# Kernel optimization log

Measured on AMD Instinct MI355X. Metric: run time of the kernel, lower is better.

The kernel has to match this reference:

```python
import jax, jax.numpy as jnp
from jax import lax
import numpy as np

IMG = 224
NB = IMG // 8  # 28 blocks per spatial dim

# DCT-II (ortho) 8x8 basis matrix
_D = np.cos(np.pi * (2 * np.arange(8)[None, :] + 1) * np.arange(8)[:, None] / 16.0) * np.sqrt(2.0 / 8.0)
_D[0, :] *= 1.0 / np.sqrt(2.0)
DCT8 = jnp.asarray(_D, dtype=jnp.float32)


def _conv(x, w, b, s):
    y = lax.conv_general_dilated(x, w, (s, s), 'SAME', dimension_numbers=('NCHW', 'OIHW', 'NCHW'))
    return y + b[None, :, None, None]


def _pool7(h):  # adaptive avg pool 56x56 -> 7x7, flatten
    B = h.shape[0]
    return h.reshape(B, 64, 7, 8, 7, 8).mean(axis=(3, 5)).reshape(B, -1)


def setup_inputs() -> dict:
    key = jax.random.key(0)
    ks = jax.random.split(key, 16)
    r = jax.nn.initializers.normal(0.02)
    inp = {
        'x': jax.random.uniform(ks[0], (64, 3, IMG, IMG), jnp.float32),
        'w_stem': r(ks[1], (64, 3, 7, 7), jnp.float32), 'b_stem': jnp.zeros((64,), jnp.float32),
        'w1': r(ks[2], (128, 64, 3, 3), jnp.float32), 'b1': jnp.zeros((128,), jnp.float32),
        'w2': r(ks[3], (256, 128, 3, 3), jnp.float32), 'b2': jnp.zeros((256,), jnp.float32),
        'w3': r(ks[4], (512, 256, 3, 3), jnp.float32), 'b3': jnp.zeros((512,), jnp.float32),
        'wd1': r(ks[5], (32, 3, 3, 3), jnp.float32), 'bd1': jnp.zeros((32,), jnp.float32),
        'wd2': r(ks[6], (64, 32, 3, 3), jnp.float32), 'bd2': jnp.zeros((64,), jnp.float32),
        'wf1': r(ks[7], (32, 6, 3, 3), jnp.float32), 'bf1': jnp.zeros((32,), jnp.float32),
        'wf2': r(ks[8], (64, 32, 3, 3), jnp.float32), 'bf2': jnp.zeros((64,), jnp.float32),
        'W_freq': r(ks[9], (6272, 512), jnp.float32), 'b_freq': jnp.zeros((512,), jnp.float32),
        'W_fu1': r(ks[10], (1024, 1024), jnp.float32), 'b_fu1': jnp.zeros((1024,), jnp.float32),
        'W_fu2': r(ks[11], (1024, 512), jnp.float32), 'b_fu2': jnp.zeros((512,), jnp.float32),
        'W_cls': r(ks[12], (512, 2), jnp.float32), 'b_cls': jnp.zeros((2,), jnp.float32),
        'temp': 1.5 * jnp.ones((1,), jnp.float32),
    }
    return inp


def reference(x, w_stem, b_stem, w1, b1, w2, b2, w3, b3, wd1, bd1, wd2, bd2,
              wf1, bf1, wf2, bf2, W_freq, b_freq, W_fu1, b_fu1, W_fu2, b_fu2,
              W_cls, b_cls, temp):
    relu = jax.nn.relu
    B = x.shape[0]
    # --- CNN backbone (resnet18 surrogate): 4 stride-2 stages -> GAP 512 ---
    h = relu(_conv(x, w_stem, b_stem, 2))
    h = relu(_conv(h, w1, b1, 2))
    h = relu(_conv(h, w2, b2, 2))
    h = relu(_conv(h, w3, b3, 2))
    backbone_feat = h.mean(axis=(2, 3))  # [B, 512]
    # --- DCT branch: grayscale -> batched 8x8 block DCT-II ortho -> mean -> resize ---
    gray = (0.299 * x[:, 0] + 0.587 * x[:, 1] + 0.114 * x[:, 2]) * 255.0  # [B,224,224]
    blocks = gray.reshape(B, NB, 8, NB, 8).transpose(0, 1, 3, 2, 4)  # [B,28,28,8,8]
    dctb = jnp.einsum('ij,bmnjk,lk->bmnil', DCT8, blocks, DCT8)  # D @ blk @ D^T
    dct_img = dctb.mean(axis=(1, 2))  # [B,8,8]
    dct_img = jax.image.resize(dct_img, (B, IMG, IMG), 'bilinear')
    dct_in = jnp.broadcast_to(dct_img[:, None], (B, 3, IMG, IMG))
    hd = relu(_conv(dct_in, wd1, bd1, 2))
    hd = relu(_conv(hd, wd2, bd2, 2))  # [B,64,56,56]
    dct_pooled = _pool7(hd)  # [B,3136]
    # --- FFT branch: batched 2D FFT, interleaved real/imag per channel -> 6 ch ---
    f = jnp.fft.fft2(x)  # [B,3,224,224] complex
    fft_in = jnp.stack([f.real, f.imag], axis=2).reshape(B, 6, IMG, IMG).astype(x.dtype)
    hf = relu(_conv(fft_in, wf1, bf1, 2))
    hf = relu(_conv(hf, wf2, bf2, 2))
    fft_pooled = _pool7(hf)  # [B,3136]
    # --- fusion + classifier + temperature scaling ---
    freq = relu(jnp.concatenate([dct_pooled, fft_pooled], axis=1) @ W_freq + b_freq)
    comb = jnp.concatenate([backbone_feat, freq], axis=1)  # [B,1024]
    fused = relu(relu(comb @ W_fu1 + b_fu1) @ W_fu2 + b_fu2)
    logits = fused @ W_cls + b_cls
    calibrated = logits / temp
    return (logits, calibrated)
```

## Files before the change

kernel.cpp:

```cpp
#include <hip/hip_runtime.h>

#ifndef M_PI
#define M_PI 3.14159265358979323846
#endif


#define BATCH 64

typedef __bf16 bf16x8 __attribute__((ext_vector_type(8)));
typedef float f32x4 __attribute__((ext_vector_type(4)));

__device__ __forceinline__ unsigned short f2bf(float f) {
    unsigned u = __float_as_uint(f);
    u += 0x7FFF + ((u >> 16) & 1);
    return (unsigned short)(u >> 16);
}
__device__ __forceinline__ unsigned packsplit(float v) {
    unsigned short h = f2bf(v);
    float hf = __uint_as_float(((unsigned)h) << 16);
    unsigned short l = f2bf(v - hf);
    return (((unsigned)h) << 16) | (unsigned)l;
}

union U8frag { bf16x8 v; unsigned d[4]; };

__device__ __forceinline__ void unpack8(const unsigned* p, bf16x8& hi, bf16x8& lo) {
    uint4 a = *(const uint4*)p;
    uint4 b = *(const uint4*)(p + 4);
    U8frag H, L;
    H.d[0] = __builtin_amdgcn_perm(a.y, a.x, 0x07060302u);
    L.d[0] = __builtin_amdgcn_perm(a.y, a.x, 0x05040100u);
    H.d[1] = __builtin_amdgcn_perm(a.w, a.z, 0x07060302u);
    L.d[1] = __builtin_amdgcn_perm(a.w, a.z, 0x05040100u);
    H.d[2] = __builtin_amdgcn_perm(b.y, b.x, 0x07060302u);
    L.d[2] = __builtin_amdgcn_perm(b.y, b.x, 0x05040100u);
    H.d[3] = __builtin_amdgcn_perm(b.w, b.z, 0x07060302u);
    L.d[3] = __builtin_amdgcn_perm(b.w, b.z, 0x05040100u);
    hi = H.v; lo = L.v;
}

__device__ __forceinline__ bf16x8 bfneg(bf16x8 v) {
    U8frag a; a.v = v;
    a.d[0] ^= 0x80008000u; a.d[1] ^= 0x80008000u;
    a.d[2] ^= 0x80008000u; a.d[3] ^= 0x80008000u;
    return a.v;
}

__device__ __forceinline__ int swz_bx() {
    int bx = blockIdx.x;
    int nb = gridDim.x;
    if ((nb & 7) == 0) bx = (bx & 7) * (nb >> 3) + (bx >> 3);
    return bx;
}

__global__ void prep_w(const float* __restrict__ w, unsigned* __restrict__ dst,
                       int Co, int Ci) {
    int idx = blockIdx.x * 256 + threadIdx.x;
    int tot = Co * Ci * 9;
    if (idx >= tot) return;
    int k9 = idx % 9;
    int rest = idx / 9;
    int ci = rest % Ci, co = rest / Ci;
    dst[((size_t)k9 * Co + co) * Ci + ci] = packsplit(w[idx]);
}

__global__ void prep_wstem(const float* __restrict__ w, unsigned* __restrict__ dst) {
    int idx = blockIdx.x * 256 + threadIdx.x;
    if (idx >= 64 * 224) return;
    int co = idx / 224, k = idx % 224;
    int ci = k & 3, kx = (k >> 2) & 7, ky = k >> 5;
    float v = 0.f;
    if (ci < 3 && kx < 7)
        v = w[((co * 3 + ci) * 7 + ky) * 7 + kx];
    dst[idx] = packsplit(v);
}

__global__ void pack_f32(const float* __restrict__ src, unsigned* __restrict__ dst, int n) {
    int i = blockIdx.x * 256 + threadIdx.x;
    if (i < n) dst[i] = packsplit(src[i]);
}

__global__ __launch_bounds__(256)
void conv3x3s2_mfma(const unsigned* __restrict__ inP, const unsigned* __restrict__ wP,
                    const float* __restrict__ bias,
                    unsigned* __restrict__ outPk, float* __restrict__ outF0,
                    float* __restrict__ outF1,
                    int Ci, int Co, int Hin, int Win, int Hout, int Wout,
                    int NTOT, int ciPer, int mode) {
    __shared__ unsigned sA[128 * 36];
    __shared__ unsigned sB[64 * 36];
    const int tid = threadIdx.x;
    const int wv = tid >> 6, lane = tid & 63;
    const int ciBeg = blockIdx.z * ciPer;
    const int coT0 = blockIdx.y * 128;
    const int HWin = Hin * Win, HWout = Hout * Wout;
    const int bx = swz_bx();

    const int nG = bx * 64 + (tid >> 2);
    const int kqB = tid & 3;
    int bb = 0, yy = 0, xx = 0;
    bool nval = nG < NTOT;
    if (nval) {
        bb = nG / HWout;
        int rem = nG - bb * HWout;
        yy = rem / Wout;
        xx = rem - yy * Wout;
    }
    const unsigned baseImg = (unsigned)bb * Ci * HWin;
    const int coA = tid >> 1, halfA = tid & 1;

    f32x4 acc[2][4];
#pragma unroll
    for (int s = 0; s < 2; s++)
#pragma unroll
        for (int t = 0; t < 4; t++) acc[s][t] = (f32x4){0.f, 0.f, 0.f, 0.f};

    for (int k9 = 0; k9 < 9; k9++) {
        int ky = k9 / 3, kx = k9 - ky * 3;
        int iy = 2 * yy + ky, ix = 2 * xx + kx;
        bool bval = nval && iy < Hin && ix < Win;
        unsigned off0 = baseImg + (unsigned)iy * Win + (unsigned)ix;
        const unsigned* wbase = wP + ((size_t)k9 * Co + coT0 + coA) * Ci + ciBeg + halfA * 16;

        for (int c0 = 0; c0 < ciPer; c0 += 32) {
            __syncthreads();
            {
                const uint4* g = (const uint4*)(wbase + c0);
                uint4 v0 = g[0], v1 = g[1], v2 = g[2], v3 = g[3];
                uint4* d = (uint4*)(sA + coA * 36 + halfA * 16);
                d[0] = v0; d[1] = v1; d[2] = v2; d[3] = v3;
            }
            {
                unsigned u[8];
                const unsigned cbase = off0 + (unsigned)(ciBeg + c0 + kqB * 8) * HWin;
#pragma unroll
                for (int j = 0; j < 8; j++)
                    u[j] = bval ? inP[cbase + (unsigned)j * HWin] : 0u;
                uint4* d = (uint4*)(sB + (tid >> 2) * 36 + kqB * 8);
                uint4 w0; w0.x = u[0]; w0.y = u[1]; w0.z = u[2]; w0.w = u[3];
                uint4 w1; w1.x = u[4]; w1.y = u[5]; w1.z = u[6]; w1.w = u[7];
                d[0] = w0; d[1] = w1;
            }
            __syncthreads();

            bf16x8 ah[2], al[2], bh[4], bl[4];
            const int m = lane & 15, q = lane >> 4;
#pragma unroll
            for (int s = 0; s < 2; s++)
                unpack8(sA + (wv * 32 + s * 16 + m) * 36 + q * 8, ah[s], al[s]);
#pragma unroll
            for (int t = 0; t < 4; t++)
                unpack8(sB + (t * 16 + m) * 36 + q * 8, bh[t], bl[t]);

#pragma unroll
            for (int s = 0; s < 2; s++)
#pragma unroll
                for (int t = 0; t < 4; t++)
                    acc[s][t] = __builtin_amdgcn_mfma_f32_16x16x32_bf16(ah[s], bh[t], acc[s][t], 0, 0, 0);
#pragma unroll
            for (int s = 0; s < 2; s++)
#pragma unroll
                for (int t = 0; t < 4; t++)
                    acc[s][t] = __builtin_amdgcn_mfma_f32_16x16x32_bf16(ah[s], bl[t], acc[s][t], 0, 0, 0);
#pragma unroll
            for (int s = 0; s < 2; s++)
#pragma unroll
                for (int t = 0; t < 4; t++)
                    acc[s][t] = __builtin_amdgcn_mfma_f32_16x16x32_bf16(al[s], bh[t], acc[s][t], 0, 0, 0);
        }
    }

    const int m = lane & 15, q = lane >> 4;
#pragma unroll
    for (int t = 0; t < 4; t++) {
        int n_g = bx * 64 + t * 16 + m;
        if (n_g >= NTOT) continue;
        int b = n_g / HWout;
        int rem = n_g - b * HWout;
        size_t nb = (size_t)b * Co * HWout + rem;
#pragma unroll
        for (int s = 0; s < 2; s++) {
            int co_l = wv * 32 + s * 16 + q * 4;
#pragma unroll
            for (int r = 0; r < 4; r++) {
                int co_g = coT0 + co_l + r;
                float v = acc[s][t][r];
                size_t addr = nb + (size_t)co_g * HWout;
                if (mode == 0) {
                    v += bias[co_g];
                    v = v > 0.f ? v : 0.f;
                    outPk[addr] = packsplit(v);
                } else {
                    (blockIdx.z == 0 ? outF0 : outF1)[addr] = v;
                }
            }
        }
    }
}

__global__ __launch_bounds__(256)
void conv3x3s2_mfma64(const unsigned* __restrict__ inP, const unsigned* __restrict__ wP,
                      const float* __restrict__ bias, float* __restrict__ outF,
                      int Hin, int Win, int Hout, int Wout, int NTOT) {
    const int Ci = 32;
    __shared__ unsigned sA[64 * 36];
    __shared__ unsigned sB[64 * 36];
    const int tid = threadIdx.x;
    const int wv = tid >> 6, lane = tid & 63;
    const int HWin = Hin * Win, HWout = Hout * Wout;
    const int bx = swz_bx();

    const int nG = bx * 64 + (tid >> 2);
    const int kq = tid & 3;
    int bb = 0, yy = 0, xx = 0;
    bool nval = nG < NTOT;
    if (nval) {
        bb = nG / HWout;
        int rem = nG - bb * HWout;
        yy = rem / Wout;
        xx = rem - yy * Wout;
    }
    const unsigned baseImg = (unsigned)bb * Ci * HWin;
    const int ch = wv & 1, nh = wv >> 1;

    f32x4 acc[2][2];
#pragma unroll
    for (int s = 0; s < 2; s++)
#pragma unroll
        for (int t = 0; t < 2; t++) acc[s][t] = (f32x4){0.f, 0.f, 0.f, 0.f};

    for (int k9 = 0; k9 < 9; k9++) {
        int ky = k9 / 3, kx = k9 - ky * 3;
        int iy = 2 * yy + ky, ix = 2 * xx + kx;
        bool bval = nval && iy < Hin && ix < Win;
        unsigned off0 = baseImg + (unsigned)iy * Win + (unsigned)ix;
        __syncthreads();
        {
            const unsigned* g = wP + ((size_t)k9 * 64 + (tid >> 2)) * Ci + kq * 8;
            uint4 v0 = *(const uint4*)g;
            uint4 v1 = *(const uint4*)(g + 4);
            uint4* d = (uint4*)(sA + (tid >> 2) * 36 + kq * 8);
            d[0] = v0; d[1] = v1;
        }
        {
            unsigned u[8];
            const unsigned cbase = off0 + (unsigned)(kq * 8) * HWin;
#pragma unroll
            for (int j = 0; j < 8; j++)
                u[j] = bval ? inP[cbase + (unsigned)j * HWin] : 0u;
            uint4* d = (uint4*)(sB + (tid >> 2) * 36 + kq * 8);
            uint4 w0; w0.x = u[0]; w0.y = u[1]; w0.z = u[2]; w0.w = u[3];
            uint4 w1; w1.x = u[4]; w1.y = u[5]; w1.z = u[6]; w1.w = u[7];
            d[0] = w0; d[1] = w1;
        }
        __syncthreads();

        bf16x8 ah[2], al[2], bh[2], bl[2];
        const int m = lane & 15, q = lane >> 4;
#pragma unroll
        for (int s = 0; s < 2; s++)
            unpack8(sA + (ch * 32 + s * 16 + m) * 36 + q * 8, ah[s], al[s]);
#pragma unroll
        for (int t = 0; t < 2; t++)
            unpack8(sB + (nh * 32 + t * 16 + m) * 36 + q * 8, bh[t], bl[t]);

#pragma unroll
        for (int s = 0; s < 2; s++)
#pragma unroll
            for (int t = 0; t < 2; t++)
                acc[s][t] = __builtin_amdgcn_mfma_f32_16x16x32_bf16(ah[s], bh[t], acc[s][t], 0, 0, 0);
#pragma unroll
        for (int s = 0; s < 2; s++)
#pragma unroll
            for (int t = 0; t < 2; t++)
                acc[s][t] = __builtin_amdgcn_mfma_f32_16x16x32_bf16(ah[s], bl[t], acc[s][t], 0, 0, 0);
#pragma unroll
        for (int s = 0; s < 2; s++)
#pragma unroll
            for (int t = 0; t < 2; t++)
                acc[s][t] = __builtin_amdgcn_mfma_f32_16x16x32_bf16(al[s], bh[t], acc[s][t], 0, 0, 0);
    }

    const int m = lane & 15, q = lane >> 4;
#pragma unroll
    for (int t = 0; t < 2; t++) {
        int n_g = bx * 64 + nh * 32 + t * 16 + m;
        if (n_g >= NTOT) continue;
        int b = n_g / HWout;
        int rem = n_g - b * HWout;
        size_t nb = (size_t)b * 64 * HWout + rem;
#pragma unroll
        for (int s = 0; s < 2; s++) {
            int co0 = ch * 32 + s * 16 + q * 4;
#pragma unroll
            for (int r = 0; r < 4; r++) {
                int co = co0 + r;
                float v = acc[s][t][r] + bias[co];
                outF[nb + (size_t)co * HWout] = v > 0.f ? v : 0.f;
            }
        }
    }
}

__global__ __launch_bounds__(256)
void conv7x7s2_mfma(const unsigned* __restrict__ inP, const unsigned* __restrict__ wP,
                    const float* __restrict__ bias, unsigned* __restrict__ outPk,
                    int NTOT) {
    __shared__ unsigned sA[64 * 36];
    __shared__ unsigned sB[64 * 36];
    const int tid = threadIdx.x;
    const int wv = tid >> 6, lane = tid & 63;
    const int HWout = 112 * 112;
    const int bx = swz_bx();

    const int nG = bx * 64 + (tid >> 2);
    const int kq = tid & 3;
    bool nval = nG < NTOT;
    int bb = 0, yy = 0, xx = 0;
    if (nval) {
        bb = nG / HWout;
        int rem = nG - bb * HWout;
        yy = rem / 112;
        xx = rem - yy * 112;
    }
    const int iy0 = 2 * yy - 2, ix0 = 2 * xx - 2;
    const unsigned baseImg = (unsigned)bb * 3 * 50176;
    const int ch = wv & 1, nh = wv >> 1;

    f32x4 acc[2][2];
#pragma unroll
    for (int s = 0; s < 2; s++)
#pragma unroll
        for (int t = 0; t < 2; t++) acc[s][t] = (f32x4){0.f, 0.f, 0.f, 0.f};

#pragma unroll
    for (int kyc = 0; kyc < 7; kyc++) {
        const int c0 = kyc * 32;
        const int iy = iy0 + kyc;
        const bool iyv = nval && iy >= 0 && iy < 224;
        __syncthreads();
        {
            const unsigned* g = wP + (tid >> 2) * 224 + c0 + kq * 8;
            uint4 v0 = *(const uint4*)g;
            uint4 v1 = *(const uint4*)(g + 4);
            uint4* d = (uint4*)(sA + (tid >> 2) * 36 + kq * 8);
            d[0] = v0; d[1] = v1;
        }
        {
            unsigned u[8];
            const unsigned rowbase = baseImg + (unsigned)(iy * 224);
#pragma unroll
            for (int j = 0; j < 8; j++) {
                int ci = j & 3;
                int kx = kq * 2 + (j >> 2);
                int ix = ix0 + kx;
                bool v = iyv && ci < 3 && kx < 7 && ix >= 0 && ix < 224;
                u[j] = v ? inP[rowbase + (unsigned)(ci * 50176 + ix)] : 0u;
            }
            uint4* d = (uint4*)(sB + (tid >> 2) * 36 + kq * 8);
            uint4 w0; w0.x = u[0]; w0.y = u[1]; w0.z = u[2]; w0.w = u[3];
            uint4 w1; w1.x = u[4]; w1.y = u[5]; w1.z = u[6]; w1.w = u[7];
            d[0] = w0; d[1] = w1;
        }
        __syncthreads();

        bf16x8 ah[2], al[2], bh[2], bl[2];
        const int m = lane & 15, q = lane >> 4;
#pragma unroll
        for (int s = 0; s < 2; s++)
            unpack8(sA + (ch * 32 + s * 16 + m) * 36 + q * 8, ah[s], al[s]);
#pragma unroll
        for (int t = 0; t < 2; t++)
            unpack8(sB + (nh * 32 + t * 16 + m) * 36 + q * 8, bh[t], bl[t]);

#pragma unroll
        for (int s = 0; s < 2; s++)
#pragma unroll
            for (int t = 0; t < 2; t++)
                acc[s][t] = __builtin_amdgcn_mfma_f32_16x16x32_bf16(ah[s], bh[t], acc[s][t], 0, 0, 0);
#pragma unroll
        for (int s = 0; s < 2; s++)
#pragma unroll
            for (int t = 0; t < 2; t++)
                acc[s][t] = __builtin_amdgcn_mfma_f32_16x16x32_bf16(ah[s], bl[t], acc[s][t], 0, 0, 0);
#pragma unroll
        for (int s = 0; s < 2; s++)
#pragma unroll
            for (int t = 0; t < 2; t++)
                acc[s][t] = __builtin_amdgcn_mfma_f32_16x16x32_bf16(al[s], bh[t], acc[s][t], 0, 0, 0);
    }

    const int m = lane & 15, q = lane >> 4;
#pragma unroll
    for (int t = 0; t < 2; t++) {
        int n_g = bx * 64 + nh * 32 + t * 16 + m;
        if (n_g >= NTOT) continue;
        int b = n_g / HWout;
        int rem = n_g - b * HWout;
        size_t nb = (size_t)b * 64 * HWout + rem;
#pragma unroll
        for (int s = 0; s < 2; s++) {
            int co0 = ch * 32 + s * 16 + q * 4;
#pragma unroll
            for (int r = 0; r < 4; r++) {
                int co = co0 + r;
                float v = acc[s][t][r] + bias[co];
                v = v > 0.f ? v : 0.f;
                outPk[nb + (size_t)co * HWout] = packsplit(v);
            }
        }
    }
}

__global__ void make_dft(unsigned* __restrict__ wre, unsigned* __restrict__ wim) {
    int idx = blockIdx.x * 256 + threadIdx.x;
    if (idx >= 224 * 224) return;
    int j = idx / 224, k = idx % 224;
    int m = (j * k) % 224;
    double a = -2.0 * M_PI * (double)m / 224.0;
    wre[idx] = packsplit((float)cos(a));
    wim[idx] = packsplit((float)sin(a));
}

__global__ void make_wsum(const float* __restrict__ wd1, float* __restrict__ wsum) {
    int idx = threadIdx.x;
    if (idx >= 288) return;
    int o = idx / 9, k = idx % 9;
    wsum[idx] = wd1[o * 27 + k] + wd1[o * 27 + 9 + k] + wd1[o * 27 + 18 + k];
}

__global__ __launch_bounds__(64)
void dft_mfma_s1(const unsigned* __restrict__ wre, const unsigned* __restrict__ wim,
                 const unsigned* __restrict__ xpk,
                 unsigned* __restrict__ ttre, unsigned* __restrict__ ttim) {
    const int z = blockIdx.z;
    const int m0 = blockIdx.x * 32, n0 = blockIdx.y * 32;
    const int lane = threadIdx.x;
    const int ml = lane & 15, q = lane >> 4;
    const unsigned* xb = xpk + (size_t)z * 50176;

    f32x4 cre[2][2], cim[2][2];
#pragma unroll
    for (int s = 0; s < 2; s++)
#pragma unroll
        for (int t = 0; t < 2; t++) { cre[s][t] = (f32x4){0,0,0,0}; cim[s][t] = (f32x4){0,0,0,0}; }

    for (int k0 = 0; k0 < 224; k0 += 32) {
        bf16x8 arh[2], arl[2], aih[2], ail[2], bh[2], bl[2];
#pragma unroll
        for (int s = 0; s < 2; s++) {
            int row = m0 + s * 16 + ml;
            unpack8(wre + row * 224 + k0 + q * 8, arh[s], arl[s]);
            unpack8(wim + row * 224 + k0 + q * 8, aih[s], ail[s]);
        }
#pragma unroll
        for (int t = 0; t < 2; t++)
            unpack8(xb + (n0 + t * 16 + ml) * 224 + k0 + q * 8, bh[t], bl[t]);

#pragma unroll
        for (int s = 0; s < 2; s++)
#pragma unroll
            for (int t = 0; t < 2; t++) {
                cre[s][t] = __builtin_amdgcn_mfma_f32_16x16x32_bf16(arh[s], bh[t], cre[s][t], 0, 0, 0);
                cre[s][t] = __builtin_amdgcn_mfma_f32_16x16x32_bf16(arh[s], bl[t], cre[s][t], 0, 0, 0);
                cre[s][t] = __builtin_amdgcn_mfma_f32_16x16x32_bf16(arl[s], bh[t], cre[s][t], 0, 0, 0);
                cim[s][t] = __builtin_amdgcn_mfma_f32_16x16x32_bf16(aih[s], bh[t], cim[s][t], 0, 0, 0);
                cim[s][t] = __builtin_amdgcn_mfma_f32_16x16x32_bf16(aih[s], bl[t], cim[s][t], 0, 0, 0);
                cim[s][t] = __builtin_amdgcn_mfma_f32_16x16x32_bf16(ail[s], bh[t], cim[s][t], 0, 0, 0);
            }
    }

    unsigned* tre = ttre + (size_t)z * 50176;
    unsigned* tim = ttim + (size_t)z * 50176;
#pragma unroll
    for (int s = 0; s < 2; s++)
#pragma unroll
        for (int t = 0; t < 2; t++)
#pragma unroll
            for (int r = 0; r < 4; r++) {
                int m = m0 + s * 16 + q * 4 + r;
                int n = n0 + t * 16 + ml;
                tre[m * 224 + n] = packsplit(cre[s][t][r]);
                tim[m * 224 + n] = packsplit(cim[s][t][r]);
            }
}

__global__ __launch_bounds__(64)
void dft_mfma_s2(const unsigned* __restrict__ wre, const unsigned* __restrict__ wim,
                 const unsigned* __restrict__ ttre, const unsigned* __restrict__ ttim,
                 float* __restrict__ fft_in) {
    const int z = blockIdx.z;
    const int m0 = blockIdx.x * 32, n0 = blockIdx.y * 32;
    const int lane = threadIdx.x;
    const int ml = lane & 15, q = lane >> 4;
    const unsigned* tre = ttre + (size_t)z * 50176;
    const unsigned* tim = ttim + (size_t)z * 50176;

    f32x4 cre[2][2], cim[2][2];
#pragma unroll
    for (int s = 0; s < 2; s++)
#pragma unroll
        for (int t = 0; t < 2; t++) { cre[s][t] = (f32x4){0,0,0,0}; cim[s][t] = (f32x4){0,0,0,0}; }

    for (int k0 = 0; k0 < 224; k0 += 32) {
        bf16x8 arh[2], arl[2], aih[2], ail[2];
        bf16x8 brh[2], brl[2], bih[2], bil[2];
#pragma unroll
        for (int s = 0; s < 2; s++) {
            int row = m0 + s * 16 + ml;
            unpack8(wre + row * 224 + k0 + q * 8, arh[s], arl[s]);
            unpack8(wim + row * 224 + k0 + q * 8, aih[s], ail[s]);
        }
#pragma unroll
        for (int t = 0; t < 2; t++) {
            int row = n0 + t * 16 + ml;
            unpack8(tre + row * 224 + k0 + q * 8, brh[t], brl[t]);
            unpack8(tim + row * 224 + k0 + q * 8, bih[t], bil[t]);
        }

#pragma unroll
        for (int t = 0; t < 2; t++) {
            bf16x8 nih = bfneg(bih[t]);
            bf16x8 nil = bfneg(bil[t]);
#pragma unroll
            for (int s = 0; s < 2; s++) {
                cre[s][t] = __builtin_amdgcn_mfma_f32_16x16x32_bf16(arh[s], brh[t], cre[s][t], 0, 0, 0);
                cre[s][t] = __builtin_amdgcn_mfma_f32_16x16x32_bf16(arh[s], brl[t], cre[s][t], 0, 0, 0);
                cre[s][t] = __builtin_amdgcn_mfma_f32_16x16x32_bf16(arl[s], brh[t], cre[s][t], 0, 0, 0);
                cre[s][t] = __builtin_amdgcn_mfma_f32_16x16x32_bf16(aih[s], nih, cre[s][t], 0, 0, 0);
                cre[s][t] = __builtin_amdgcn_mfma_f32_16x16x32_bf16(aih[s], nil, cre[s][t], 0, 0, 0);
                cre[s][t] = __builtin_amdgcn_mfma_f32_16x16x32_bf16(ail[s], nih, cre[s][t], 0, 0, 0);
                cim[s][t] = __builtin_amdgcn_mfma_f32_16x16x32_bf16(arh[s], bih[t], cim[s][t], 0, 0, 0);
                cim[s][t] = __builtin_amdgcn_mfma_f32_16x16x32_bf16(arh[s], bil[t], cim[s][t], 0, 0, 0);
                cim[s][t] = __builtin_amdgcn_mfma_f32_16x16x32_bf16(arl[s], bih[t], cim[s][t], 0, 0, 0);
                cim[s][t] = __builtin_amdgcn_mfma_f32_16x16x32_bf16(aih[s], brh[t], cim[s][t], 0, 0, 0);
                cim[s][t] = __builtin_amdgcn_mfma_f32_16x16x32_bf16(aih[s], brl[t], cim[s][t], 0, 0, 0);
                cim[s][t] = __builtin_amdgcn_mfma_f32_16x16x32_bf16(ail[s], brh[t], cim[s][t], 0, 0, 0);
            }
        }
    }

    const int b_loc = z / 3, c = z % 3;
    float* yre = fft_in + (size_t)(b_loc * 6 + 2 * c) * 50176;
    float* yim = yre + 50176;
#pragma unroll
    for (int s = 0; s < 2; s++)
#pragma unroll
        for (int t = 0; t < 2; t++)
#pragma unroll
            for (int r = 0; r < 4; r++) {
                int m = m0 + s * 16 + q * 4 + r;
                int n = n0 + t * 16 + ml;
                yre[m * 224 + n] = cre[s][t][r];
                yim[m * 224 + n] = cim[s][t][r];
            }
}

template <int CO_BLK, int TH, int TW, int CI_CHUNK, bool PACK>
__global__ __launch_bounds__(CO_BLK * TH)
void conv3x3_s2(const float* __restrict__ in, const float* __restrict__ w,
                const float* __restrict__ bias, float* __restrict__ out,
                int Ci, int Co, int Hin, int Win, int Hout, int Wout) {
    constexpr int IN_H = 2 * TH + 1;
    constexpr int IN_W = 2 * TW + 1;
    constexpr int IN_WP = 32;
    constexpr int WSTR = (CI_CHUNK * 9) | 1;
    __shared__ __align__(16) float s_in[CI_CHUNK][IN_H][IN_WP];
    __shared__ float s_w[CO_BLK * WSTR];

    const int tid = threadIdx.x;
    const int tiles_x = Wout / TW;
    const int tile = blockIdx.x;
    const int ty0 = (tile / tiles_x) * TH;
    const int tx0 = (tile % tiles_x) * TW;
    const int cog = blockIdx.y;
    const int b = blockIdx.z;
    const int co = tid % CO_BLK;
    const int ty = tid / CO_BLK;
    const int co_g = cog * CO_BLK + co;

    float acc[TW];
#pragma unroll
    for (int i = 0; i < TW; i++) acc[i] = 0.f;

    const float* in_b = in + (size_t)b * Ci * Hin * Win;
    const int iy0 = 2 * ty0, ix0 = 2 * tx0;

    for (int ci0 = 0; ci0 < Ci; ci0 += CI_CHUNK) {
        for (int idx = tid; idx < CI_CHUNK * IN_H * IN_W; idx += CO_BLK * TH) {
            int ci = idx / (IN_H * IN_W);
            int rem = idx % (IN_H * IN_W);
            int r = rem / IN_W, cc = rem % IN_W;
            int gy = iy0 + r, gx = ix0 + cc;
            float v = 0.f;
            if (gy < Hin && gx < Win)
                v = in_b[(size_t)(ci0 + ci) * Hin * Win + (size_t)gy * Win + gx];
            s_in[ci][r][cc] = v;
        }
        for (int idx = tid; idx < CO_BLK * CI_CHUNK * 9; idx += CO_BLK * TH) {
            int c = idx / (CI_CHUNK * 9);
            int k = idx % (CI_CHUNK * 9);
            s_w[c * WSTR + k] = w[((size_t)(cog * CO_BLK + c) * Ci + ci0) * 9 + k];
        }
        __syncthreads();

#pragma unroll
        for (int ci = 0; ci < CI_CHUNK; ci++) {
            float wr[9];
#pragma unroll
            for (int k = 0; k < 9; k++) wr[k] = s_w[co * WSTR + ci * 9 + k];
#pragma unroll
            for (int ky = 0; ky < 3; ky++) {
                float r[IN_WP];
                const float4* rowp = (const float4*)&s_in[ci][2 * ty + ky][0];
#pragma unroll
                for (int qq = 0; qq < IN_WP / 4; qq++) {
                    float4 v = rowp[qq];
                    r[4 * qq] = v.x; r[4 * qq + 1] = v.y; r[4 * qq + 2] = v.z; r[4 * qq + 3] = v.w;
                }
#pragma unroll
                for (int kx = 0; kx < 3; kx++) {
                    float wv = wr[ky * 3 + kx];
#pragma unroll
                    for (int xq = 0; xq < TW; xq++) acc[xq] += r[2 * xq + kx] * wv;
                }
            }
        }
        __syncthreads();
    }
    float bb = bias[co_g];
    size_t obase = ((size_t)b * Co + co_g) * Hout * Wout + (size_t)(ty0 + ty) * Wout + tx0;
#pragma unroll
    for (int xq = 0; xq < TW; xq++) {
        float v = acc[xq] + bb;
        v = v > 0.f ? v : 0.f;
        if (PACK)
            ((unsigned*)out)[obase + xq] = packsplit(v);
        else
            out[obase + xq] = v;
    }
}

__device__ __forceinline__ float dct_coef(int u, int i) {
    if (u == 0) return 0.35355339059327373f;
    return 0.5f * cosf((float)M_PI * (float)((2 * i + 1) * u) / 16.0f);
}

__global__ __launch_bounds__(256)
void dct_partial(const float* __restrict__ x, float* __restrict__ accum) {
    __shared__ float red[256];
    const int b = blockIdx.x, g = blockIdx.y;
    const int tid = threadIdx.x;
    const int ij = tid & 63;
    const int grp = tid >> 6;
    const int i = ij >> 3, j = ij & 7;
    const float* xb = x + (size_t)b * 3 * 50176;
    float s = 0.f;
    for (int blk = g * 4 + grp; blk < 784; blk += 48) {
        int m = blk / 28, n = blk % 28;
        size_t o = (size_t)(m * 8 + i) * 224 + n * 8 + j;
        s += 0.299f * xb[o] + 0.587f * xb[50176 + o] + 0.114f * xb[2 * 50176 + o];
    }
    red[tid] = s;
    __syncthreads();
    if (tid < 64)
        atomicAdd(&accum[b * 64 + tid],
                  red[tid] + red[tid + 64] + red[tid + 128] + red[tid + 192]);
}

__global__ __launch_bounds__(64)
void dct_final(const float* __restrict__ accum, float* __restrict__ dct_out) {
    __shared__ float Mb[64];
    const int b = blockIdx.x, tid = threadIdx.x;
    Mb[tid] = accum[b * 64 + tid] * (255.f / 784.f);
    __syncthreads();
    int u = tid >> 3, v = tid & 7;
    float acc = 0.f;
#pragma unroll
    for (int i2 = 0; i2 < 8; i2++) {
        float du = dct_coef(u, i2);
#pragma unroll
        for (int j2 = 0; j2 < 8; j2++) acc += du * Mb[i2 * 8 + j2] * dct_coef(v, j2);
    }
    dct_out[b * 64 + tid] = acc;
}

__global__ void resize_bilinear(const float* __restrict__ dct, float* __restrict__ out) {
    int idx = blockIdx.x * 256 + threadIdx.x;
    if (idx >= BATCH * 224 * 224) return;
    int b = idx / (224 * 224);
    int rem = idx % (224 * 224);
    int y = rem / 224, xx = rem % 224;
    float sy = fminf(fmaxf((y + 0.5f) * (1.f / 28.f) - 0.5f, 0.f), 7.f);
    float sx = fminf(fmaxf((xx + 0.5f) * (1.f / 28.f) - 0.5f, 0.f), 7.f);
    int y0 = (int)floorf(sy); if (y0 > 6) y0 = 6;
    int x0 = (int)floorf(sx); if (x0 > 6) x0 = 6;
    float ty = sy - y0, tx = sx - x0;
    const float* M = dct + b * 64;
    float v00 = M[y0 * 8 + x0], v01 = M[y0 * 8 + x0 + 1];
    float v10 = M[(y0 + 1) * 8 + x0], v11 = M[(y0 + 1) * 8 + x0 + 1];
    out[idx] = (1.f - ty) * ((1.f - tx) * v00 + tx * v01) + ty * ((1.f - tx) * v10 + tx * v11);
}

__global__ void pool7(const float* __restrict__ h, float* __restrict__ out,
                      int col_base, int n) {
    int idx = blockIdx.x * 256 + threadIdx.x;
    if (idx >= n) return;
    int b = idx / (64 * 49);
    int rem = idx % (64 * 49);
    int c = rem / 49;
    int ij = rem % 49;
    int i = ij / 7, j = ij % 7;
    const float* hp = h + ((size_t)(b * 64 + c)) * 56 * 56 + (size_t)i * 8 * 56 + j * 8;
    float s = 0.f;
#pragma unroll
    for (int r = 0; r < 8; r++)
#pragma unroll
        for (int q = 0; q < 8; q++) s += hp[r * 56 + q];
    out[(size_t)b * 6272 + col_base + c * 49 + ij] = s * (1.f / 64.f);
}

__global__ void gap2_kernel(const float* __restrict__ ha, const float* __restrict__ hb,
                            const float* __restrict__ bias, float* __restrict__ comb,
                            int nwaves) {
    int gt = blockIdx.x * blockDim.x + threadIdx.x;
    int wid = gt >> 6;
    int lane = gt & 63;
    if (wid >= nwaves) return;
    int b = wid / 512, c = wid % 512;
    const float* pa = ha + (size_t)wid * 196;
    const float* pb = hb + (size_t)wid * 196;
    float bbv = bias[c];
    float s = 0.f;
    for (int i = lane; i < 196; i += 64) {
        float v = pa[i] + pb[i] + bbv;
        s += v > 0.f ? v : 0.f;
    }
#pragma unroll
    for (int off = 32; off > 0; off >>= 1) s += __shfl_down(s, off);
    if (lane == 0) comb[(size_t)b * 1024 + c] = s * (1.f / 196.f);
}

__global__ __launch_bounds__(256)
void gemm64_part(const float* __restrict__ A, const float* __restrict__ Bm,
                 float* __restrict__ part, int N, int K, int KC) {
    __shared__ __align__(16) float sA[16][68];
    __shared__ __align__(16) float sB[16][68];
    const int tid = threadIdx.x;
    const int n0 = blockIdx.x * 64;
    const int kbase = blockIdx.z * KC;
    const int tr = (tid >> 4) << 2;
    const int tc = (tid & 15) << 2;
    float acc[4][4];
#pragma unroll
    for (int r = 0; r < 4; r++)
#pragma unroll
        for (int c = 0; c < 4; c++) acc[r][c] = 0.f;

    for (int k0 = 0; k0 < KC; k0 += 16) {
        for (int i = tid; i < 1024; i += 256) {
            int m = i >> 4, k = i & 15;
            sA[k][m] = A[(size_t)m * K + kbase + k0 + k];
        }
        for (int i = tid; i < 1024; i += 256) {
            int k = i >> 6, n = i & 63;
            sB[k][n] = Bm[(size_t)(kbase + k0 + k) * N + n0 + n];
        }
        __syncthreads();
#pragma unroll
        for (int k = 0; k < 16; k++) {
            float4 a = *(const float4*)&sA[k][tr];
            float4 bv = *(const float4*)&sB[k][tc];
            float av[4] = {a.x, a.y, a.z, a.w};
            float bb[4] = {bv.x, bv.y, bv.z, bv.w};
#pragma unroll
            for (int r = 0; r < 4; r++)
#pragma unroll
                for (int c = 0; c < 4; c++) acc[r][c] += av[r] * bb[c];
        }
        __syncthreads();
    }
    float* dst = part + (size_t)blockIdx.z * 64 * N;
#pragma unroll
    for (int r = 0; r < 4; r++) {
        float4 v; v.x = acc[r][0]; v.y = acc[r][1]; v.z = acc[r][2]; v.w = acc[r][3];
        *(float4*)&dst[(size_t)(tr + r) * N + n0 + tc] = v;
    }
}

__global__ void reduce_bias_relu(const float* __restrict__ part, const float* __restrict__ bias,
                                 float* __restrict__ dst, int N, int nz,
                                 int dstStride, int dstOff) {
    int idx = blockIdx.x * 256 + threadIdx.x;
    if (idx >= BATCH * N) return;
    int b = idx / N, n = idx % N;
    float s = bias[n];
    for (int z = 0; z < nz; z++) s += part[((size_t)z * BATCH + b) * N + n];
    dst[(size_t)b * dstStride + dstOff + n] = s > 0.f ? s : 0.f;
}

__global__ void logits_kernel(const float* __restrict__ fused, const float* __restrict__ Wc,
                              const float* __restrict__ bcls, const float* __restrict__ temp,
                              float* __restrict__ out) {
    int idx = threadIdx.x;
    if (idx >= 128) return;
    int b = idx >> 1, n = idx & 1;
    float s = bcls[n];
    const float* f = fused + (size_t)b * 512;
    for (int k = 0; k < 512; k++) s += f[k] * Wc[k * 2 + n];
    out[idx] = s;
    out[128 + idx] = s / temp[0];
}

static inline int ceil8(int n) { return (n + 7) & ~7; }

extern "C" void kernel_launch(void* const* d_in, const int* in_sizes, int n_in,
                              void* d_out, int out_size, void* d_ws, size_t ws_size,
                              hipStream_t stream) {
    const float* x      = (const float*)d_in[0];
    const float* w_stem = (const float*)d_in[1];
    const float* b_stem = (const float*)d_in[2];
    const float* w1 = (const float*)d_in[3];   const float* b1 = (const float*)d_in[4];
    const float* w2 = (const float*)d_in[5];   const float* b2 = (const float*)d_in[6];
    const float* w3 = (const float*)d_in[7];   const float* b3 = (const float*)d_in[8];
    const float* wd1 = (const float*)d_in[9];  const float* bd1 = (const float*)d_in[10];
    const float* wd2 = (const float*)d_in[11]; const float* bd2 = (const float*)d_in[12];
    const float* wf1 = (const float*)d_in[13]; const float* bf1 = (const float*)d_in[14];
    const float* wf2 = (const float*)d_in[15]; const float* bf2 = (const float*)d_in[16];
    const float* W_freq = (const float*)d_in[17]; const float* b_freq = (const float*)d_in[18];
    const float* W_fu1  = (const float*)d_in[19]; const float* b_fu1  = (const float*)d_in[20];
    const float* W_fu2  = (const float*)d_in[21]; const float* b_fu2  = (const float*)d_in[22];
    const float* W_cls  = (const float*)d_in[23]; const float* b_cls  = (const float*)d_in[24];
    const float* temp   = (const float*)d_in[25];
    float* ws = (float*)d_ws;
    float* out = (float*)d_out;

    const size_t IMG2 = 224 * 224;

    size_t oWRE  = 0;
    size_t oWIM  = oWRE + IMG2;
    size_t oWSUM = oWIM + IMG2;
    size_t oDCT  = oWSUM + 288;
    size_t oDIMG = oDCT + (size_t)BATCH * 64;
    size_t oFREQIN  = oDIMG + (size_t)BATCH * IMG2;
    size_t oCOMB    = oFREQIN + (size_t)BATCH * 6272;
    size_t oFREQACC = oCOMB + (size_t)BATCH * 1024;
    size_t oFU1     = oFREQACC + (size_t)BATCH * 512;
    size_t oFUSED   = oFU1 + (size_t)BATCH * 1024;
    size_t oDCTACC  = oFUSED + (size_t)BATCH * 512;
    size_t oW1s     = oDCTACC + (size_t)BATCH * 64;
    size_t oW2s     = oW1s + 73728;
    size_t oW3s     = oW2s + 294912;
    size_t oWF2s    = oW3s + 1179648;
    size_t oWD2s    = oWF2s + 18432;
    size_t oWSTEMs  = oWD2s + 18432;
    size_t P        = oWSTEMs + 14336;

    int CB = 16;
    while (CB > 1 && (P + (size_t)CB * 1605632) * 4 > ws_size) CB >>= 1;
    size_t base   = P;
    size_t oXPK   = base;
    size_t oSTEMP = base + (size_t)CB * 150528;
    size_t oC1P   = oSTEMP + (size_t)CB * 802816;
    size_t oC2P   = oC1P + (size_t)CB * 401408;
    size_t oC3a   = base;
    size_t oC3b   = base + (size_t)CB * 100352;
    size_t oTTRE  = oSTEMP;
    size_t oTTIM  = oSTEMP + (size_t)CB * 150528;
    size_t oFFTIN = oSTEMP + (size_t)CB * 301056;
    size_t oBIG1  = oC1P;
    size_t oBIG2  = oC2P;
    size_t oPART  = base;
    int zfreq = (CB >= 2) ? 98 : 49;
    int kcfreq = 6272 / zfreq;

    unsigned* WREp = (unsigned*)(ws + oWRE);
    unsigned* WIMp = (unsigned*)(ws + oWIM);
    unsigned* W1s = (unsigned*)(ws + oW1s);
    unsigned* W2s = (unsigned*)(ws + oW2s);
    unsigned* W3s = (unsigned*)(ws + oW3s);
    unsigned* WF2s = (unsigned*)(ws + oWF2s);
    unsigned* WD2s = (unsigned*)(ws + oWD2s);
    unsigned* WSTEMs = (unsigned*)(ws + oWSTEMs);
    unsigned* STEMP = (unsigned*)(ws + oSTEMP);
    unsigned* C1P   = (unsigned*)(ws + oC1P);
    unsigned* C2P   = (unsigned*)(ws + oC2P);
    unsigned* XPK   = (unsigned*)(ws + oXPK);
    unsigned* TTRE  = (unsigned*)(ws + oTTRE);
    unsigned* TTIM  = (unsigned*)(ws + oTTIM);
    unsigned* BIG1P = (unsigned*)(ws + oBIG1);
    float* PART = ws + oPART;

    hipMemsetAsync(ws + oDCTACC, 0, (size_t)BATCH * 64 * sizeof(float), stream);
    make_dft<<<196, 256, 0, stream>>>(WREp, WIMp);
    make_wsum<<<1, 288, 0, stream>>>(wd1, ws + oWSUM);
    prep_w<<<(128 * 64 * 9 + 255) / 256, 256, 0, stream>>>(w1, W1s, 128, 64);
    prep_w<<<(256 * 128 * 9 + 255) / 256, 256, 0, stream>>>(w2, W2s, 256, 128);
    prep_w<<<(512 * 256 * 9 + 255) / 256, 256, 0, stream>>>(w3, W3s, 512, 256);
    prep_w<<<(64 * 32 * 9 + 255) / 256, 256, 0, stream>>>(wf2, WF2s, 64, 32);
    prep_w<<<(64 * 32 * 9 + 255) / 256, 256, 0, stream>>>(wd2, WD2s, 64, 32);
    prep_wstem<<<(64 * 224 + 255) / 256, 256, 0, stream>>>(w_stem, WSTEMs);
    dct_partial<<<dim3(BATCH, 12), 256, 0, stream>>>(x, ws + oDCTACC);
    dct_final<<<BATCH, 64, 0, stream>>>(ws + oDCTACC, ws + oDCT);
    resize_bilinear<<<12544, 256, 0, stream>>>(ws + oDCT, ws + oDIMG);

    for (int b0 = 0; b0 < BATCH; b0 += CB) {
        const float* xc = x + (size_t)b0 * 3 * IMG2;
        pack_f32<<<(CB * 3 * (int)IMG2 + 255) / 256, 256, 0, stream>>>(
            xc, XPK, CB * 3 * (int)IMG2);
        dft_mfma_s1<<<dim3(7, 7, 3 * CB), 64, 0, stream>>>(WREp, WIMp, XPK, TTRE, TTIM);
        dft_mfma_s2<<<dim3(7, 7, 3 * CB), 64, 0, stream>>>(WREp, WIMp, TTRE, TTIM, ws + oFFTIN);
        conv3x3_s2<32, 8, 14, 6, true><<<dim3(112, 1, CB), 256, 0, stream>>>(
            ws + oFFTIN, wf1, bf1, ws + oBIG1, 6, 32, 224, 224, 112, 112);
        conv3x3s2_mfma64<<<dim3(ceil8(CB * 3136 / 64), 1, 1), 256, 0, stream>>>(
            BIG1P, WF2s, bf2, ws + oBIG2, 112, 112, 56, 56, CB * 3136);
        pool7<<<(CB * 64 * 49 + 255) / 256, 256, 0, stream>>>(
            ws + oBIG2, ws + oFREQIN + (size_t)b0 * 6272, 3136, CB * 64 * 49);
        conv3x3_s2<32, 8, 14, 1, true><<<dim3(112, 1, CB), 256, 0, stream>>>(
            ws + oDIMG + (size_t)b0 * IMG2, ws + oWSUM, bd1, ws + oBIG1, 1, 32, 224, 224, 112, 112);
        conv3x3s2_mfma64<<<dim3(ceil8(CB * 3136 / 64), 1, 1), 256, 0, stream>>>(
            BIG1P, WD2s, bd2, ws + oBIG2, 112, 112, 56, 56, CB * 3136);
        pool7<<<(CB * 64 * 49 + 255) / 256, 256, 0, stream>>>(
            ws + oBIG2, ws + oFREQIN + (size_t)b0 * 6272, 0, CB * 64 * 49);
        conv7x7s2_mfma<<<dim3(ceil8(CB * 196), 1, 1), 256, 0, stream>>>(
            XPK, WSTEMs, b_stem, STEMP, CB * 12544);
        conv3x3s2_mfma<<<dim3(ceil8((CB * 3136 + 63) / 64), 1, 1), 256, 0, stream>>>(
            STEMP, W1s, b1, C1P, nullptr, nullptr,
            64, 128, 112, 112, 56, 56, CB * 3136, 64, 0);
        conv3x3s2_mfma<<<dim3(ceil8((CB * 784 + 63) / 64), 2, 1), 256, 0, stream>>>(
            C1P, W2s, b2, C2P, nullptr, nullptr,
            128, 256, 56, 56, 28, 28, CB * 784, 128, 0);
        conv3x3s2_mfma<<<dim3(ceil8((CB * 196 + 63) / 64), 4, 2), 256, 0, stream>>>(
            C2P, W3s, b3, nullptr, ws + oC3a, ws + oC3b,
            256, 512, 28, 28, 14, 14, CB * 196, 128, 1);
        gap2_kernel<<<(CB * 512 * 64 + 255) / 256, 256, 0, stream>>>(
            ws + oC3a, ws + oC3b, b3, ws + oCOMB + (size_t)b0 * 1024, CB * 512);
    }

    gemm64_part<<<dim3(8, 1, zfreq), 256, 0, stream>>>(ws + oFREQIN, W_freq, PART,
                                                       512, 6272, kcfreq);
    reduce_bias_relu<<<128, 256, 0, stream>>>(PART, b_freq, ws + oCOMB, 512, zfreq, 1024, 512);
    gemm64_part<<<dim3(16, 1, 16), 256, 0, stream>>>(ws + oCOMB, W_fu1, PART,
                                                     1024, 1024, 64);
    reduce_bias_relu<<<256, 256, 0, stream>>>(PART, b_fu1, ws + oFU1, 1024, 16, 1024, 0);
    gemm64_part<<<dim3(8, 1, 16), 256, 0, stream>>>(ws + oFU1, W_fu2, PART,
                                                    512, 1024, 64);
    reduce_bias_relu<<<128, 256, 0, stream>>>(PART, b_fu2, ws + oFUSED, 512, 16, 512, 0);
    logits_kernel<<<1, 128, 0, stream>>>(ws + oFUSED, W_cls, b_cls, temp, out);
}
```

Measured before the change: 1.872 ms.

## Register-prefetch next K-chunk of global loads to overlap with MFMA compute in convs

In the three implicit-GEMM conv kernels (general stride-2 conv, 64-output conv, and 7x7 stem), global loads for the next K iteration are issued into registers right after the LDS barrier, so they overlap with the current iteration's unpack and MFMA work. The nested k9/c0 loop is flattened into a single iteration counter so the prefetch can cross kernel-tap boundaries. This hides global memory latency that was previously exposed between barriers, at the cost of extra live registers, which may lower occupancy.

```diff
diff --git a/kernel.cpp b/kernel.cpp
--- a/kernel.cpp
+++ b/kernel.cpp
@@ -108,66 +108,75 @@
     }
     const unsigned baseImg = (unsigned)bb * Ci * HWin;
     const int coA = tid >> 1, halfA = tid & 1;
-
-    f32x4 acc[2][4];
-#pragma unroll
-    for (int s = 0; s < 2; s++)
-#pragma unroll
-        for (int t = 0; t < 4; t++) acc[s][t] = (f32x4){0.f, 0.f, 0.f, 0.f};
-
-    for (int k9 = 0; k9 < 9; k9++) {
+    const int nc = ciPer >> 5;
+    const int T = 9 * nc;
+
+    uint4 ra[4];
+    unsigned rb[8];
+    auto loadIter = [&](int it) {
+        int k9 = it / nc;
+        int c0 = (it - k9 * nc) << 5;
         int ky = k9 / 3, kx = k9 - ky * 3;
         int iy = 2 * yy + ky, ix = 2 * xx + kx;
         bool bval = nval && iy < Hin && ix < Win;
         unsigned off0 = baseImg + (unsigned)iy * Win + (unsigned)ix;
-        const unsigned* wbase = wP + ((size_t)k9 * Co + coT0 + coA) * Ci + ciBeg + halfA * 16;
-
-        for (int c0 = 0; c0 < ciPer; c0 += 32) {
-            __syncthreads();
-            {
-                const uint4* g = (const uint4*)(wbase + c0);
-                uint4 v0 = g[0], v1 = g[1], v2 = g[2], v3 = g[3];
-                uint4* d = (uint4*)(sA + coA * 36 + halfA * 16);
-                d[0] = v0; d[1] = v1; d[2] = v2; d[3] = v3;
-            }
-            {
-                unsigned u[8];
-                const unsigned cbase = off0 + (unsigned)(ciBeg + c0 + kqB * 8) * HWin;
-#pragma unroll
-                for (int j = 0; j < 8; j++)
-                    u[j] = bval ? inP[cbase + (unsigned)j * HWin] : 0u;
-                uint4* d = (uint4*)(sB + (tid >> 2) * 36 + kqB * 8);
-                uint4 w0; w0.x = u[0]; w0.y = u[1]; w0.z = u[2]; w0.w = u[3];
-                uint4 w1; w1.x = u[4]; w1.y = u[5]; w1.z = u[6]; w1.w = u[7];
-                d[0] = w0; d[1] = w1;
-            }
-            __syncthreads();
-
-            bf16x8 ah[2], al[2], bh[4], bl[4];
-            const int m = lane & 15, q = lane >> 4;
-#pragma unroll
-            for (int s = 0; s < 2; s++)
-                unpack8(sA + (wv * 32 + s * 16 + m) * 36 + q * 8, ah[s], al[s]);
+        const unsigned* wb = wP + ((size_t)k9 * Co + coT0 + coA) * Ci + ciBeg + c0 + halfA * 16;
+        ra[0] = *(const uint4*)wb;
+        ra[1] = *(const uint4*)(wb + 4);
+        ra[2] = *(const uint4*)(wb + 8);
+        ra[3] = *(const uint4*)(wb + 12);
+        const unsigned cbase = off0 + (unsigned)(ciBeg + c0 + kqB * 8) * HWin;
+#pragma unroll
+        for (int j = 0; j < 8; j++)
+            rb[j] = bval ? inP[cbase + (unsigned)j * HWin] : 0u;
+    };
+
+    f32x4 acc[2][4];
+#pragma unroll
+    for (int s = 0; s < 2; s++)
+#pragma unroll
+        for (int t = 0; t < 4; t++) acc[s][t] = (f32x4){0.f, 0.f, 0.f, 0.f};
+
+    loadIter(0);
+    for (int it = 0; it < T; it++) {
+        __syncthreads();
+        {
+            uint4* d = (uint4*)(sA + coA * 36 + halfA * 16);
+            d[0] = ra[0]; d[1] = ra[1]; d[2] = ra[2]; d[3] = ra[3];
+        }
+        {
+            uint4* d = (uint4*)(sB + (tid >> 2) * 36 + kqB * 8);
+            uint4 w0; w0.x = rb[0]; w0.y = rb[1]; w0.z = rb[2]; w0.w = rb[3];
+            uint4 w1; w1.x = rb[4]; w1.y = rb[5]; w1.z = rb[6]; w1.w = rb[7];
+            d[0] = w0; d[1] = w1;
+        }
+        __syncthreads();
+        if (it + 1 < T) loadIter(it + 1);
+
+        bf16x8 ah[2], al[2], bh[4], bl[4];
+        const int m = lane & 15, q = lane >> 4;
+#pragma unroll
+        for (int s = 0; s < 2; s++)
+            unpack8(sA + (wv * 32 + s * 16 + m) * 36 + q * 8, ah[s], al[s]);
+#pragma unroll
+        for (int t = 0; t < 4; t++)
+            unpack8(sB + (t * 16 + m) * 36 + q * 8, bh[t], bl[t]);
+
+#pragma unroll
+        for (int s = 0; s < 2; s++)
 #pragma unroll
             for (int t = 0; t < 4; t++)
-                unpack8(sB + (t * 16 + m) * 36 + q * 8, bh[t], bl[t]);
-
-#pragma unroll
-            for (int s = 0; s < 2; s++)
-#pragma unroll
-                for (int t = 0; t < 4; t++)
-                    acc[s][t] = __builtin_amdgcn_mfma_f32_16x16x32_bf16(ah[s], bh[t], acc[s][t], 0, 0, 0);
-#pragma unroll
-            for (int s = 0; s < 2; s++)
-#pragma unroll
-                for (int t = 0; t < 4; t++)
-                    acc[s][t] = __builtin_amdgcn_mfma_f32_16x16x32_bf16(ah[s], bl[t], acc[s][t], 0, 0, 0);
-#pragma unroll
-            for (int s = 0; s < 2; s++)
-#pragma unroll
-                for (int t = 0; t < 4; t++)
-                    acc[s][t] = __builtin_amdgcn_mfma_f32_16x16x32_bf16(al[s], bh[t], acc[s][t], 0, 0, 0);
-        }
+                acc[s][t] = __builtin_amdgcn_mfma_f32_16x16x32_bf16(ah[s], bh[t], acc[s][t], 0, 0, 0);
+#pragma unroll
+        for (int s = 0; s < 2; s++)
+#pragma unroll
+            for (int t = 0; t < 4; t++)
+                acc[s][t] = __builtin_amdgcn_mfma_f32_16x16x32_bf16(ah[s], bl[t], acc[s][t], 0, 0, 0);
+#pragma unroll
+        for (int s = 0; s < 2; s++)
+#pragma unroll
+            for (int t = 0; t < 4; t++)
+                acc[s][t] = __builtin_amdgcn_mfma_f32_16x16x32_bf16(al[s], bh[t], acc[s][t], 0, 0, 0);
     }
 
     const int m = lane & 15, q = lane >> 4;
@@ -223,37 +232,43 @@
     const unsigned baseImg = (unsigned)bb * Ci * HWin;
     const int ch = wv & 1, nh = wv >> 1;
 
-    f32x4 acc[2][2];
-#pragma unroll
-    for (int s = 0; s < 2; s++)
-#pragma unroll
-        for (int t = 0; t < 2; t++) acc[s][t] = (f32x4){0.f, 0.f, 0.f, 0.f};
-
-    for (int k9 = 0; k9 < 9; k9++) {
+    uint4 ra[2];
+    unsigned rb[8];
+    auto loadIter = [&](int k9) {
         int ky = k9 / 3, kx = k9 - ky * 3;
         int iy = 2 * yy + ky, ix = 2 * xx + kx;
         bool bval = nval && iy < Hin && ix < Win;
         unsigned off0 = baseImg + (unsigned)iy * Win + (unsigned)ix;
+        const unsigned* g = wP + ((size_t)k9 * 64 + (tid >> 2)) * Ci + kq * 8;
+        ra[0] = *(const uint4*)g;
+        ra[1] = *(const uint4*)(g + 4);
+        const unsigned cbase = off0 + (unsigned)(kq * 8) * HWin;
+#pragma unroll
+        for (int j = 0; j < 8; j++)
+            rb[j] = bval ? inP[cbase + (unsigned)j * HWin] : 0u;
+    };
+
+    f32x4 acc[2][2];
+#pragma unroll
+    for (int s = 0; s < 2; s++)
+#pragma unroll
+        for (int t = 0; t < 2; t++) acc[s][t] = (f32x4){0.f, 0.f, 0.f, 0.f};
+
+    loadIter(0);
+    for (int k9 = 0; k9 < 9; k9++) {
         __syncthreads();
         {
-            const unsigned* g = wP + ((size_t)k9 * 64 + (tid >> 2)) * Ci + kq * 8;
-            uint4 v0 = *(const uint4*)g;
-            uint4 v1 = *(const uint4*)(g + 4);
             uint4* d = (uint4*)(sA + (tid >> 2) * 36 + kq * 8);
-            d[0] = v0; d[1] = v1;
+            d[0] = ra[0]; d[1] = ra[1];
         }
         {
-            unsigned u[8];
-            const unsigned cbase = off0 + (unsigned)(kq * 8) * HWin;
-#pragma unroll
-            for (int j = 0; j < 8; j++)
-                u[j] = bval ? inP[cbase + (unsigned)j * HWin] : 0u;
             uint4* d = (uint4*)(sB + (tid >> 2) * 36 + kq * 8);
-            uint4 w0; w0.x = u[0]; w0.y = u[1]; w0.z = u[2]; w0.w = u[3];
-            uint4 w1; w1.x = u[4]; w1.y = u[5]; w1.z = u[6]; w1.w = u[7];
+            uint4 w0; w0.x = rb[0]; w0.y = rb[1]; w0.z = rb[2]; w0.w = rb[3];
+            uint4 w1; w1.x = rb[4]; w1.y = rb[5]; w1.z = rb[6]; w1.w = rb[7];
             d[0] = w0; d[1] = w1;
         }
         __syncthreads();
+        if (k9 + 1 < 9) loadIter(k9 + 1);
 
         bf16x8 ah[2], al[2], bh[2], bl[2];
         const int m = lane & 15, q = lane >> 4;
@@ -327,42 +342,47 @@
     const unsigned baseImg = (unsigned)bb * 3 * 50176;
     const int ch = wv & 1, nh = wv >> 1;
 
-    f32x4 acc[2][2];
-#pragma unroll
-    for (int s = 0; s < 2; s++)
-#pragma unroll
-        for (int t = 0; t < 2; t++) acc[s][t] = (f32x4){0.f, 0.f, 0.f, 0.f};
-
-#pragma unroll
-    for (int kyc = 0; kyc < 7; kyc++) {
+    uint4 ra[2];
+    unsigned rb[8];
+    auto loadIter = [&](int kyc) {
         const int c0 = kyc * 32;
         const int iy = iy0 + kyc;
         const bool iyv = nval && iy >= 0 && iy < 224;
+        const unsigned* g = wP + (tid >> 2) * 224 + c0 + kq * 8;
+        ra[0] = *(const uint4*)g;
+        ra[1] = *(const uint4*)(g + 4);
+        const unsigned rowbase = baseImg + (unsigned)(iy * 224);
+#pragma unroll
+        for (int j = 0; j < 8; j++) {
+            int ci = j & 3;
+            int kx = kq * 2 + (j >> 2);
+            int ix = ix0 + kx;
+            bool v = iyv && ci < 3 && kx < 7 && ix >= 0 && ix < 224;
+            rb[j] = v ? inP[rowbase + (unsigned)(ci * 50176 + ix)] : 0u;
+        }
+    };
+
+    f32x4 acc[2][2];
+#pragma unroll
+    for (int s = 0; s < 2; s++)
+#pragma unroll
+        for (int t = 0; t < 2; t++) acc[s][t] = (f32x4){0.f, 0.f, 0.f, 0.f};
+
+    loadIter(0);
+    for (int kyc = 0; kyc < 7; kyc++) {
         __syncthreads();
         {
-            const unsigned* g = wP + (tid >> 2) * 224 + c0 + kq * 8;
-            uint4 v0 = *(const uint4*)g;
-            uint4 v1 = *(const uint4*)(g + 4);
             uint4* d = (uint4*)(sA + (tid >> 2) * 36 + kq * 8);
-            d[0] = v0; d[1] = v1;
+            d[0] = ra[0]; d[1] = ra[1];
         }
         {
-            unsigned u[8];
-            const unsigned rowbase = baseImg + (unsigned)(iy * 224);
-#pragma unroll
-            for (int j = 0; j < 8; j++) {
-                int ci = j & 3;
-                int kx = kq * 2 + (j >> 2);
-                int ix = ix0 + kx;
-                bool v = iyv && ci < 3 && kx < 7 && ix >= 0 && ix < 224;
-                u[j] = v ? inP[rowbase + (unsigned)(ci * 50176 + ix)] : 0u;
-            }
             uint4* d = (uint4*)(sB + (tid >> 2) * 36 + kq * 8);
-            uint4 w0; w0.x = u[0]; w0.y = u[1]; w0.z = u[2]; w0.w = u[3];
-            uint4 w1; w1.x = u[4]; w1.y = u[5]; w1.z = u[6]; w1.w = u[7];
+            uint4 w0; w0.x = rb[0]; w0.y = rb[1]; w0.z = rb[2]; w0.w = rb[3];
+            uint4 w1; w1.x = rb[4]; w1.y = rb[5]; w1.z = rb[6]; w1.w = rb[7];
             d[0] = w0; d[1] = w1;
         }
         __syncthreads();
+        if (kyc + 1 < 7) loadIter(kyc + 1);
 
         bf16x8 ah[2], al[2], bh[2], bl[2];
         const int m = lane & 15, q = lane >> 4;
```

After: 2.736 ms. +46.2%, slower.
